# Kernel optimization log

Measured on AMD Instinct MI355X. Metric: run time of the kernel, lower is better.

## Reference

```python
import jax, jax.numpy as jnp
import numpy as np
import math

# static configuration
SPATIAL_SHAPES = [(100, 150), (50, 75), (25, 38), (13, 19)]  # (H, W) per level
EMBED, HEADS, LEVELS, POINTS = 256, 8, 4, 4
HEAD_DIM = EMBED // HEADS
BS = 2
NV = sum(h * w for h, w in SPATIAL_SHAPES)  # 19947
NQ = NV  # encoder-style self-attention (value = query)


def _offset_bias():
    # replicate torch _init_weights grid init for sampling_offsets bias
    thetas = np.arange(HEADS, dtype=np.float32) * (2.0 * math.pi / HEADS)
    grid = np.stack([np.cos(thetas), np.sin(thetas)], -1)  # [H,2]
    grid = grid / np.abs(grid).max(-1, keepdims=True)
    grid = np.tile(grid[:, None, None, :], (1, LEVELS, POINTS, 1))
    for i in range(POINTS):
        grid[:, :, i, :] *= (i + 1)
    return jnp.asarray(grid.reshape(-1), dtype=jnp.float32)


def setup_inputs() -> dict:
    key = jax.random.key(0)
    ks = jax.random.split(key, 8)
    sc = 1.0 / math.sqrt(EMBED)
    return {
        "query": jax.random.normal(ks[0], (BS, NQ, EMBED), jnp.float32),
        "reference_points": jax.random.uniform(ks[1], (BS, NQ, LEVELS, 2), jnp.float32),
        "spatial_shapes": jnp.asarray(SPATIAL_SHAPES, dtype=jnp.int32),
        "W_off": jax.random.normal(ks[2], (EMBED, HEADS * LEVELS * POINTS * 2), jnp.float32) * 0.01,
        "b_off": _offset_bias(),
        "W_attn": jax.random.normal(ks[3], (EMBED, HEADS * LEVELS * POINTS), jnp.float32) * 0.01,
        "b_attn": jnp.zeros((HEADS * LEVELS * POINTS,), jnp.float32),
        "W_val": jax.random.normal(ks[4], (EMBED, EMBED), jnp.float32) * sc,
        "b_val": jnp.zeros((EMBED,), jnp.float32),
        "W_out": jax.random.normal(ks[5], (EMBED, EMBED), jnp.float32) * sc,
        "b_out": jnp.zeros((EMBED,), jnp.float32),
    }


def _bilinear_sample(value_l, loc_l, H, W):
    # value_l: [bs, H*W, heads, hd]; loc_l: [bs, nq, heads, P, 2] normalized coords
    # grid_sample semantics: align_corners=False, padding_mode='zeros'
    x = loc_l[..., 0] * W - 0.5
    y = loc_l[..., 1] * H - 0.5
    x0 = jnp.floor(x)
    y0 = jnp.floor(y)
    dx = x - x0
    dy = y - y0
    x0i = x0.astype(jnp.int32)
    y0i = y0.astype(jnp.int32)

    def gather(xi, yi):
        valid = (xi >= 0) & (xi < W) & (yi >= 0) & (yi < H)  # [bs,nq,h,P]
        idx = jnp.clip(yi, 0, H - 1) * W + jnp.clip(xi, 0, W - 1)
        bs, nq, h, P = idx.shape
        idx2 = idx.transpose(0, 1, 3, 2).reshape(bs, nq * P, h)[..., None]
        v = jnp.take_along_axis(value_l, idx2, axis=1)  # [bs, nq*P, h, hd]
        v = v.reshape(bs, nq, P, h, -1).transpose(0, 1, 3, 2, 4)  # [bs,nq,h,P,hd]
        return v * valid[..., None]

    w00 = ((1 - dx) * (1 - dy))[..., None]
    w01 = (dx * (1 - dy))[..., None]
    w10 = ((1 - dx) * dy)[..., None]
    w11 = (dx * dy)[..., None]
    return (gather(x0i, y0i) * w00 + gather(x0i + 1, y0i) * w01
            + gather(x0i, y0i + 1) * w10 + gather(x0i + 1, y0i + 1) * w11)


def reference(query, reference_points, spatial_shapes, W_off, b_off, W_attn, b_attn,
              W_val, b_val, W_out, b_out):
    bs, nq, _ = query.shape
    # value = query (encoder self-attn), identity = query
    value = (query @ W_val + b_val).reshape(bs, NV, HEADS, HEAD_DIM)
    offs = (query @ W_off + b_off).reshape(bs, nq, HEADS, LEVELS, POINTS, 2)
    attw = jax.nn.softmax((query @ W_attn + b_attn).reshape(bs, nq, HEADS, LEVELS * POINTS), axis=-1)
    attw = attw.reshape(bs, nq, HEADS, LEVELS, POINTS)
    # offset normalizer: (W, H) per level
    norm = jnp.stack([spatial_shapes[:, 1], spatial_shapes[:, 0]], -1).astype(query.dtype)
    loc = reference_points[:, :, None, :, None, :] + offs / norm[None, None, None, :, None, :]

    out = jnp.zeros((bs, nq, HEADS, HEAD_DIM), query.dtype)
    start = 0
    for lvl, (H, W) in enumerate(SPATIAL_SHAPES):
        value_l = value[:, start:start + H * W]  # static slice
        start += H * W
        sampled = _bilinear_sample(value_l, loc[:, :, :, lvl], H, W)  # [bs,nq,h,P,hd]
        out = out + jnp.einsum('bnhpc,bnhp->bnhc', sampled, attw[:, :, :, lvl, :])

    out = out.reshape(bs, nq, EMBED) @ W_out + b_out
    return out + query  # dropout(p=0) + identity
```

## Files before the change

kernel.cpp:

```cpp
#include <hip/hip_runtime.h>
#include <math.h>

#define HEADS     8
#define LEVELS    4
#define POINTS    4
#define HEAD_DIM  32
#define EMBED     256
#define NQ        19947
#define NV        19947
#define BS        2
#define M_ROWS    (BS * NQ)

typedef _Float16 h8 __attribute__((ext_vector_type(8)));
typedef _Float16 h4 __attribute__((ext_vector_type(4)));
typedef _Float16 h2 __attribute__((ext_vector_type(2)));
typedef float    f32x4 __attribute__((ext_vector_type(4)));
typedef unsigned short ushort8 __attribute__((ext_vector_type(8)));

static __device__ __forceinline__ int lvl_H(int l) {
    constexpr int v[4] = {100, 50, 25, 13}; return v[l];
}
static __device__ __forceinline__ int lvl_W(int l) {
    constexpr int v[4] = {150, 75, 38, 19}; return v[l];
}
static __device__ __forceinline__ int lvl_start(int l) {
    constexpr int v[4] = {0, 15000, 18750, 19700}; return v[l];
}

static __device__ __forceinline__ unsigned short f2h(float f) {
    _Float16 h = (_Float16)f;
    return __builtin_bit_cast(unsigned short, h);
}

static __device__ __forceinline__ void gload_lds16(const void* g, void* l) {
    __builtin_amdgcn_global_load_lds(
        (const __attribute__((address_space(1))) void*)g,
        (__attribute__((address_space(3))) void*)l, 16, 0, 0);
}

static __device__ __forceinline__ void pkacc_s(h2* acc, uint4 u, _Float16 w) {
    const h2 wv = {w, w};
    acc[0] = __builtin_bit_cast(h2, u.x) * wv + acc[0];
    acc[1] = __builtin_bit_cast(h2, u.y) * wv + acc[1];
    acc[2] = __builtin_bit_cast(h2, u.z) * wv + acc[2];
    acc[3] = __builtin_bit_cast(h2, u.w) * wv + acc[3];
}

__global__ __launch_bounds__(256) void pack_query_kernel(
    const float* __restrict__ query, unsigned short* __restrict__ qh)
{
    const int tid = blockIdx.x * 256 + threadIdx.x;
    if (tid >= M_ROWS * 32) return;
    const int row = tid >> 5;
    const int k8  = tid & 31;
    const float* src = query + (size_t)row * 256 + k8 * 8;
    const float4 v0 = *(const float4*)(src);
    const float4 v1 = *(const float4*)(src + 4);
    ushort8 o;
    o[0] = f2h(v0.x); o[1] = f2h(v0.y); o[2] = f2h(v0.z); o[3] = f2h(v0.w);
    o[4] = f2h(v1.x); o[5] = f2h(v1.y); o[6] = f2h(v1.z); o[7] = f2h(v1.w);
    const int g  = k8 >> 3;
    const int u2 = (k8 & 7) ^ (row & 7);
    *(ushort8*)((char*)qh + (size_t)row * 512 + g * 128 + u2 * 16) = o;
}

__global__ __launch_bounds__(256) void pack_weights_kernel(
    const float* __restrict__ Wv, const float* __restrict__ Wo,
    const float* __restrict__ Wa, const float* __restrict__ Wout,
    unsigned short* __restrict__ Wcat, unsigned short* __restrict__ WoutT)
{
    const int tid = blockIdx.x * 256 + threadIdx.x;
    if (tid >= 896 * 32) return;
    const int row = tid >> 5;
    const int k8  = tid & 31;
    const float* src; int n_local, N; unsigned short* dstb; int r_local;
    if (row < 256)      { src = Wv;   n_local = row;       N = 256; dstb = Wcat;  r_local = row; }
    else if (row < 512) { src = Wo;   n_local = row - 256; N = 256; dstb = Wcat;  r_local = row; }
    else if (row < 640) { src = Wa;   n_local = row - 512; N = 128; dstb = Wcat;  r_local = row; }
    else                { src = Wout; n_local = row - 640; N = 256; dstb = WoutT; r_local = row - 640; }
    const int k = k8 * 8;
    ushort8 o;
    #pragma unroll
    for (int j = 0; j < 8; ++j)
        o[j] = f2h(src[(size_t)(k + j) * N + n_local]);
    const int g  = k8 >> 3;
    const int u2 = (k8 & 7) ^ (r_local & 7);
    *(ushort8*)((char*)dstb + (size_t)r_local * 512 + g * 128 + u2 * 16) = o;
}

template <int EPI>
__global__ __launch_bounds__(256) void mfma_gemm_kernel(
    const unsigned short* __restrict__ Ah,
    const unsigned short* __restrict__ Bh,
    unsigned short* __restrict__ value_h,
    unsigned short* __restrict__ oa,
    const float* __restrict__ b_val, const float* __restrict__ b_off,
    const float* __restrict__ b_attn,
    const float* __restrict__ b_out, const float* __restrict__ query,
    float* __restrict__ out)
{
    __shared__ alignas(16) char As[16384];
    __shared__ alignas(16) char Bs[16384];

    const int t    = threadIdx.x;
    const int wid  = t >> 6;
    const int lane = t & 63;
    const int l15  = lane & 15;
    const int lhi  = lane >> 4;
    const int wr   = wid >> 1;
    const int wc   = wid & 1;
    const int m0   = blockIdx.x * 128;
    const int n0   = blockIdx.y * 128;

    f32x4 acc[4][4] = {};

    auto stage = [&](int ks) {
        #pragma unroll
        for (int j = 0; j < 4; ++j) {
            const int q  = j * 256 + wid * 64 + lane;
            const int tr = q >> 3;
            const int u  = q & 7;
            int gr = m0 + tr; gr = gr < M_ROWS ? gr : (M_ROWS - 1);
            gload_lds16((const char*)Ah + (size_t)gr * 512 + ks * 128 + u * 16,
                        As + (j * 256 + wid * 64) * 16);
            const int gn = n0 + tr;
            gload_lds16((const char*)Bh + (size_t)gn * 512 + ks * 128 + u * 16,
                        Bs + (j * 256 + wid * 64) * 16);
        }
    };

    stage(0);
    for (int ks = 0; ks < 4; ++ks) {
        __syncthreads();
        #pragma unroll
        for (int kc = 0; kc < 2; ++kc) {
            h8 a[4], b[4];
            #pragma unroll
            for (int i = 0; i < 4; ++i) {
                const int tr = wr * 64 + i * 16 + l15;
                const int ua = (kc * 4 + lhi) ^ (tr & 7);
                a[i] = *(const h8*)&As[tr * 128 + ua * 16];
                const int tn = wc * 64 + i * 16 + l15;
                const int ub = (kc * 4 + lhi) ^ (tn & 7);
                b[i] = *(const h8*)&Bs[tn * 128 + ub * 16];
            }
            #pragma unroll
            for (int i = 0; i < 4; ++i)
                #pragma unroll
                for (int j2 = 0; j2 < 4; ++j2)
                    acc[i][j2] = __builtin_amdgcn_mfma_f32_16x16x32_f16(
                        a[i], b[j2], acc[i][j2], 0, 0, 0);
        }
        if (ks < 3) { __syncthreads(); stage(ks + 1); }
    }

    if (EPI == 0) {
        const int by = blockIdx.y;
        if (by < 2) {
            #pragma unroll
            for (int j2 = 0; j2 < 4; ++j2) {
                const int gn = n0 + wc * 64 + j2 * 16 + l15;
                const float bias = b_val[gn];
                const int h = gn >> 5, ch = gn & 31;
                #pragma unroll
                for (int i = 0; i < 4; ++i) {
                    #pragma unroll
                    for (int r = 0; r < 4; ++r) {
                        const int gm = m0 + wr * 64 + i * 16 + lhi * 4 + r;
                        if (gm >= M_ROWS) continue;
                        const int bb  = gm >= NQ;
                        const int pix = gm - bb * NQ;
                        value_h[(((size_t)bb * 8 + h) * NV + pix) * 32 + ch] =
                            f2h(acc[i][j2][r] + bias);
                    }
                }
            }
        } else {
            #pragma unroll
            for (int j2 = 0; j2 < 4; ++j2) {
                const int gn  = n0 + wc * 64 + j2 * 16 + l15;
                const int col = gn - 256;
                const float bias = (col < 256) ? b_off[col] : b_attn[col - 256];
                #pragma unroll
                for (int i = 0; i < 4; ++i) {
                    #pragma unroll
                    for (int r = 0; r < 4; ++r) {
                        const int gm = m0 + wr * 64 + i * 16 + lhi * 4 + r;
                        if (gm >= M_ROWS) continue;
                        oa[(size_t)gm * 384 + col] = f2h(acc[i][j2][r] + bias);
                    }
                }
            }
        }
    } else {
        #pragma unroll
        for (int j2 = 0; j2 < 4; ++j2) {
            const int gn = n0 + wc * 64 + j2 * 16 + l15;
            const float bias = b_out[gn];
            #pragma unroll
            for (int i = 0; i < 4; ++i) {
                #pragma unroll
                for (int r = 0; r < 4; ++r) {
                    const int gm = m0 + wr * 64 + i * 16 + lhi * 4 + r;
                    if (gm >= M_ROWS) continue;
                    out[(size_t)gm * 256 + gn] =
                        acc[i][j2][r] + bias + query[(size_t)gm * 256 + gn];
                }
            }
        }
    }
}

__global__ __launch_bounds__(256) void sample_kernel_v12(
    const unsigned short* __restrict__ value,
    const _Float16* __restrict__ oa,
    const float* __restrict__ refp,
    unsigned short* __restrict__ outa_h)
{
    __shared__ uint4 sw_lds[16][65];

    const int bx    = blockIdx.x;
    const int h     = bx & 7;
    const int chunk = bx >> 3;
    const int g     = threadIdx.x >> 2;
    const int q     = threadIdx.x & 3;
    const int row   = chunk * 64 + g;
    const bool valid = row < M_ROWS;

    if (valid) {
        const int lvl = q;
        const _Float16* oar = oa + (size_t)row * 384;
        const h8 oxy = *(const h8*)(oar + h * 32 + lvl * 8);
        const h4 lgh = *(const h4*)(oar + 256 + h * 16 + lvl * 4);
        const float lg0 = (float)lgh[0], lg1 = (float)lgh[1];
        const float lg2 = (float)lgh[2], lg3 = (float)lgh[3];

        float mx = fmaxf(fmaxf(lg0, lg1), fmaxf(lg2, lg3));
        mx = fmaxf(mx, __shfl_xor(mx, 1));
        mx = fmaxf(mx, __shfl_xor(mx, 2));
        const float e0 = expf(lg0 - mx);
        const float e1 = expf(lg1 - mx);
        const float e2 = expf(lg2 - mx);
        const float e3 = expf(lg3 - mx);
        float sum = e0 + e1 + e2 + e3;
        sum += __shfl_xor(sum, 1);
        sum += __shfl_xor(sum, 2);
        const float inv = 1.f / sum;

        const float2 rr = *(const float2*)(refp + (size_t)row * 8 + lvl * 2);
        const int W = lvl_W(lvl), H = lvl_H(lvl), st = lvl_start(lvl);
        const float rx = rr.x * (float)W - 0.5f;
        const float ry = rr.y * (float)H - 0.5f;

        const float sxv[4] = {(float)oxy[0] + rx, (float)oxy[2] + rx,
                              (float)oxy[4] + rx, (float)oxy[6] + rx};
        const float syv[4] = {(float)oxy[1] + ry, (float)oxy[3] + ry,
                              (float)oxy[5] + ry, (float)oxy[7] + ry};
        const float ev[4]  = {e0 * inv, e1 * inv, e2 * inv, e3 * inv};

        #pragma unroll
        for (int p = 0; p < 4; ++p) {
            const float cx = sxv[p], cy = syv[p], wz = ev[p];
            const float fx = floorf(cx), fy = floorf(cy);
            const int x0 = (int)fx, y0 = (int)fy;
            const float dx = cx - fx, dy = cy - fy;
            const float omx = 1.f - dx, omy = 1.f - dy;
            float w00 = omx * omy * wz;
            float w01 = dx  * omy * wz;
            float w10 = omx * dy  * wz;
            float w11 = dx  * dy  * wz;
            const bool vx0 = (unsigned)x0       < (unsigned)W;
            const bool vx1 = (unsigned)(x0 + 1) < (unsigned)W;
            const bool vy0 = (unsigned)y0       < (unsigned)H;
            const bool vy1 = (unsigned)(y0 + 1) < (unsigned)H;
            w00 = (vx0 & vy0) ? w00 : 0.f;
            w01 = (vx1 & vy0) ? w01 : 0.f;
            w10 = (vx0 & vy1) ? w10 : 0.f;
            w11 = (vx1 & vy1) ? w11 : 0.f;
            const int xs0 = min(max(x0, 0), W - 1);
            const int xs1 = min(max(x0 + 1, 0), W - 1);
            const int ys0 = min(max(y0, 0), H - 1);
            const int ys1 = min(max(y0 + 1, 0), H - 1);
            const int r0i = st + ys0 * W;
            const int r1i = st + ys1 * W;
            uint4 e;
            e.x = ((unsigned)(r0i + xs1) << 16) | (unsigned)(r0i + xs0);
            e.y = ((unsigned)(r1i + xs1) << 16) | (unsigned)(r1i + xs0);
            e.z = ((unsigned)f2h(w01) << 16) | (unsigned)f2h(w00);
            e.w = ((unsigned)f2h(w11) << 16) | (unsigned)f2h(w10);
            sw_lds[lvl * 4 + p][g] = e;
        }
    }
    __syncthreads();
    if (!valid) return;

    const int b = row >= NQ;
    const char* vb = (const char*)value + (((size_t)b * 8 + h) * NV) * 64 + q * 16;

    h2 acc[4] = {};
    #pragma unroll
    for (int s = 0; s < 16; ++s) {
        const uint4 e = sw_lds[s][g];
        const h2 wA = __builtin_bit_cast(h2, e.z);
        const h2 wB = __builtin_bit_cast(h2, e.w);
        const uint4 u00 = *(const uint4*)(vb + ((size_t)(e.x & 0xffffu) << 6));
        const uint4 u01 = *(const uint4*)(vb + ((size_t)(e.x >> 16)     << 6));
        const uint4 u10 = *(const uint4*)(vb + ((size_t)(e.y & 0xffffu) << 6));
        const uint4 u11 = *(const uint4*)(vb + ((size_t)(e.y >> 16)     << 6));
        pkacc_s(acc, u00, wA[0]);
        pkacc_s(acc, u01, wA[1]);
        pkacc_s(acc, u10, wB[0]);
        pkacc_s(acc, u11, wB[1]);
    }

    const int bytecol = h * 64 + q * 16;
    const int g2 = bytecol >> 7;
    const int u2 = ((bytecol >> 4) & 7) ^ (row & 7);
    uint4 d;
    d.x = __builtin_bit_cast(unsigned, acc[0]);
    d.y = __builtin_bit_cast(unsigned, acc[1]);
    d.z = __builtin_bit_cast(unsigned, acc[2]);
    d.w = __builtin_bit_cast(unsigned, acc[3]);
    *(uint4*)((char*)outa_h + (size_t)row * 512 + g2 * 128 + u2 * 16) = d;
}

extern "C" void kernel_launch(void* const* d_in, const int* in_sizes, int n_in,
                              void* d_out, int out_size, void* d_ws, size_t ws_size,
                              hipStream_t stream)
{
    const float* query  = (const float*)d_in[0];
    const float* refp   = (const float*)d_in[1];
    const float* W_off  = (const float*)d_in[3];
    const float* b_off  = (const float*)d_in[4];
    const float* W_attn = (const float*)d_in[5];
    const float* b_attn = (const float*)d_in[6];
    const float* W_val  = (const float*)d_in[7];
    const float* b_val  = (const float*)d_in[8];
    const float* W_out  = (const float*)d_in[9];
    const float* b_out  = (const float*)d_in[10];
    float* out = (float*)d_out;

    char* p = (char*)d_ws;
    unsigned short* qh    = (unsigned short*)p;
    unsigned short* oah   = qh;
    p += (size_t)M_ROWS * 512;
    unsigned short* value_h = (unsigned short*)p;  p += (size_t)M_ROWS * 512;
    unsigned short* Wcat  = (unsigned short*)p;  p += (size_t)640 * 512;
    unsigned short* WoutT = (unsigned short*)p;  p += (size_t)256 * 512;
    unsigned short* oa = (unsigned short*)p;  p += (size_t)M_ROWS * 384 * 2;

    const dim3 blk(256);

    pack_query_kernel<<<(M_ROWS * 32 + 255) / 256, blk, 0, stream>>>(query, qh);
    pack_weights_kernel<<<(896 * 32 + 255) / 256, blk, 0, stream>>>(
        W_val, W_off, W_attn, W_out, Wcat, WoutT);

    const dim3 g1((M_ROWS + 127) / 128, 5);
    mfma_gemm_kernel<0><<<g1, blk, 0, stream>>>(
        qh, Wcat, value_h, oa, b_val, b_off, b_attn,
        nullptr, nullptr, nullptr);

    const int chunks = (M_ROWS + 63) / 64;
    sample_kernel_v12<<<chunks * 8, blk, 0, stream>>>(
        value_h, (const _Float16*)oa, refp, oah);

    const dim3 g2((M_ROWS + 127) / 128, 2);
    mfma_gemm_kernel<1><<<g2, blk, 0, stream>>>(
        oah, WoutT, nullptr, nullptr, nullptr, nullptr, nullptr,
        b_out, query, out);
}
```

Before: 158.5 us.

## Sample bilinear corners as contiguous pixel pairs with 8 lanes per query

The sampling kernel now treats the two horizontally adjacent bilinear corners as one 128-byte contiguous span. Eight lanes split it, so each lane issues two 16-byte loads per sample instead of four, with the x index clamped to W-2 and the corner weights folded into low and high slots. Lane halves select their weight with a byte permute, and partial sums are combined by a cross-lane shuffle before four lanes write the result. This halves rows per block and doubles the grid, aiming for more memory-level parallelism and fewer load instructions, at the cost of the extra shuffle and idle lanes during weight setup.

```diff
diff --git a/kernel.cpp b/kernel.cpp
--- a/kernel.cpp
+++ b/kernel.cpp
@@ -38,8 +38,8 @@
         (__attribute__((address_space(3))) void*)l, 16, 0, 0);
 }
 
-static __device__ __forceinline__ void pkacc_s(h2* acc, uint4 u, _Float16 w) {
-    const h2 wv = {w, w};
+static __device__ __forceinline__ void pkacc_u(h2* acc, uint4 u, unsigned wbits) {
+    const h2 wv = __builtin_bit_cast(h2, wbits);
     acc[0] = __builtin_bit_cast(h2, u.x) * wv + acc[0];
     acc[1] = __builtin_bit_cast(h2, u.y) * wv + acc[1];
     acc[2] = __builtin_bit_cast(h2, u.z) * wv + acc[2];
@@ -211,24 +211,24 @@
     }
 }
 
-__global__ __launch_bounds__(256) void sample_kernel_v12(
+__global__ __launch_bounds__(256) void sample_kernel_v13(
     const unsigned short* __restrict__ value,
     const _Float16* __restrict__ oa,
     const float* __restrict__ refp,
     unsigned short* __restrict__ outa_h)
 {
-    __shared__ uint4 sw_lds[16][65];
+    __shared__ uint4 sw_lds[16][34];
 
     const int bx    = blockIdx.x;
     const int h     = bx & 7;
     const int chunk = bx >> 3;
-    const int g     = threadIdx.x >> 2;
-    const int q     = threadIdx.x & 3;
-    const int row   = chunk * 64 + g;
+    const int g     = threadIdx.x >> 3;
+    const int l8    = threadIdx.x & 7;
+    const int row   = chunk * 32 + g;
     const bool valid = row < M_ROWS;
 
-    if (valid) {
-        const int lvl = q;
+    if (valid && l8 < 4) {
+        const int lvl = l8;
         const _Float16* oar = oa + (size_t)row * 384;
         const h8 oxy = *(const h8*)(oar + h * 32 + lvl * 8);
         const h4 lgh = *(const h4*)(oar + 256 + h * 16 + lvl * 4);
@@ -277,17 +277,22 @@
             w01 = (vx1 & vy0) ? w01 : 0.f;
             w10 = (vx0 & vy1) ? w10 : 0.f;
             w11 = (vx1 & vy1) ? w11 : 0.f;
+            const int px  = min(max(x0, 0), W - 2);
             const int xs0 = min(max(x0, 0), W - 1);
             const int xs1 = min(max(x0 + 1, 0), W - 1);
+            const float wlo0 = (xs0 == px ? w00 : 0.f) + (xs1 == px ? w01 : 0.f);
+            const float whi0 = (xs0 == px + 1 ? w00 : 0.f) + (xs1 == px + 1 ? w01 : 0.f);
+            const float wlo1 = (xs0 == px ? w10 : 0.f) + (xs1 == px ? w11 : 0.f);
+            const float whi1 = (xs0 == px + 1 ? w10 : 0.f) + (xs1 == px + 1 ? w11 : 0.f);
             const int ys0 = min(max(y0, 0), H - 1);
             const int ys1 = min(max(y0 + 1, 0), H - 1);
-            const int r0i = st + ys0 * W;
-            const int r1i = st + ys1 * W;
+            const unsigned pix0 = (unsigned)(st + ys0 * W + px);
+            const unsigned pix1 = (unsigned)(st + ys1 * W + px);
             uint4 e;
-            e.x = ((unsigned)(r0i + xs1) << 16) | (unsigned)(r0i + xs0);
-            e.y = ((unsigned)(r1i + xs1) << 16) | (unsigned)(r1i + xs0);
-            e.z = ((unsigned)f2h(w01) << 16) | (unsigned)f2h(w00);
-            e.w = ((unsigned)f2h(w11) << 16) | (unsigned)f2h(w10);
+            e.x = pix0 | (pix1 << 16);
+            e.y = ((unsigned)f2h(whi0) << 16) | (unsigned)f2h(wlo0);
+            e.z = ((unsigned)f2h(whi1) << 16) | (unsigned)f2h(wlo1);
+            e.w = 0;
             sw_lds[lvl * 4 + p][g] = e;
         }
     }
@@ -295,33 +300,39 @@
     if (!valid) return;
 
     const int b = row >= NQ;
-    const char* vb = (const char*)value + (((size_t)b * 8 + h) * NV) * 64 + q * 16;
+    const char* vb = (const char*)value + (((size_t)b * 8 + h) * NV) * 64 + l8 * 16;
+    const unsigned selw = 0x01000100u + (unsigned)(l8 >> 2) * 0x02020202u;
 
     h2 acc[4] = {};
     #pragma unroll
     for (int s = 0; s < 16; ++s) {
         const uint4 e = sw_lds[s][g];
-        const h2 wA = __builtin_bit_cast(h2, e.z);
-        const h2 wB = __builtin_bit_cast(h2, e.w);
-        const uint4 u00 = *(const uint4*)(vb + ((size_t)(e.x & 0xffffu) << 6));
-        const uint4 u01 = *(const uint4*)(vb + ((size_t)(e.x >> 16)     << 6));
-        const uint4 u10 = *(const uint4*)(vb + ((size_t)(e.y & 0xffffu) << 6));
-        const uint4 u11 = *(const uint4*)(vb + ((size_t)(e.y >> 16)     << 6));
-        pkacc_s(acc, u00, wA[0]);
-        pkacc_s(acc, u01, wA[1]);
-        pkacc_s(acc, u10, wB[0]);
-        pkacc_s(acc, u11, wB[1]);
-    }
-
-    const int bytecol = h * 64 + q * 16;
-    const int g2 = bytecol >> 7;
-    const int u2 = ((bytecol >> 4) & 7) ^ (row & 7);
-    uint4 d;
-    d.x = __builtin_bit_cast(unsigned, acc[0]);
-    d.y = __builtin_bit_cast(unsigned, acc[1]);
-    d.z = __builtin_bit_cast(unsigned, acc[2]);
-    d.w = __builtin_bit_cast(unsigned, acc[3]);
-    *(uint4*)((char*)outa_h + (size_t)row * 512 + g2 * 128 + u2 * 16) = d;
+        const uint4 u0 = *(const uint4*)(vb + ((size_t)(e.x & 0xffffu) << 6));
+        const uint4 u1 = *(const uint4*)(vb + ((size_t)(e.x >> 16)     << 6));
+        const unsigned w0 = __builtin_amdgcn_perm(e.y, e.y, selw);
+        const unsigned w1 = __builtin_amdgcn_perm(e.z, e.z, selw);
+        pkacc_u(acc, u0, w0);
+        pkacc_u(acc, u1, w1);
+    }
+
+    #pragma unroll
+    for (int i = 0; i < 4; ++i) {
+        const unsigned a = __builtin_bit_cast(unsigned, acc[i]);
+        const unsigned o = (unsigned)__shfl_xor((int)a, 4);
+        acc[i] = acc[i] + __builtin_bit_cast(h2, o);
+    }
+
+    if (l8 < 4) {
+        const int bytecol = h * 64 + l8 * 16;
+        const int g2 = bytecol >> 7;
+        const int u2 = ((bytecol >> 4) & 7) ^ (row & 7);
+        uint4 d;
+        d.x = __builtin_bit_cast(unsigned, acc[0]);
+        d.y = __builtin_bit_cast(unsigned, acc[1]);
+        d.z = __builtin_bit_cast(unsigned, acc[2]);
+        d.w = __builtin_bit_cast(unsigned, acc[3]);
+        *(uint4*)((char*)outa_h + (size_t)row * 512 + g2 * 128 + u2 * 16) = d;
+    }
 }
 
 extern "C" void kernel_launch(void* const* d_in, const int* in_sizes, int n_in,
@@ -360,8 +371,8 @@
         qh, Wcat, value_h, oa, b_val, b_off, b_attn,
         nullptr, nullptr, nullptr);
 
-    const int chunks = (M_ROWS + 63) / 64;
-    sample_kernel_v12<<<chunks * 8, blk, 0, stream>>>(
+    const int chunks = (M_ROWS + 31) / 32;
+    sample_kernel_v13<<<chunks * 8, blk, 0, stream>>>(
         value_h, (const _Float16*)oa, refp, oah);
 
     const dim3 g2((M_ROWS + 127) / 128, 2);
```

Measured after the change: 156.4 us. Within noise of the previous version (-1.4%).
